# Kernel optimization log

Hardware: AMD Instinct MI355X
Metric: run time of the kernel (lower is better)

Reference implementation:

```python
import jax, jax.numpy as jnp
import numpy as np

N_NODES, N_EDGES, D_IN, D_H, N_GRAPHS = 50000, 600000, 1024, 128, 1000


def _transformer_conv(x, src, dst, wq, bq, wk, bk, wv, bv, ws, bs, n):
    """PyG TransformerConv, heads=1, concat=True, root_weight=True."""
    q = x @ wq + bq                      # [N, d]
    k = x @ wk + bk
    v = x @ wv + bv
    d = q.shape[-1]
    # per-edge attention score for edge j->i: <q_i, k_j> / sqrt(d)
    score = jnp.sum(q[dst] * k[src], axis=-1) / jnp.sqrt(jnp.asarray(d, x.dtype))  # [E]
    # segment softmax over incoming edges of each destination node
    smax = jax.ops.segment_max(score, dst, num_segments=n)
    smax = jnp.where(jnp.isfinite(smax), smax, jnp.zeros_like(smax))
    ex = jnp.exp(score - smax[dst])
    denom = jax.ops.segment_sum(ex, dst, num_segments=n)
    alpha = ex / (denom[dst] + 1e-16)
    # scatter-aggregate weighted values back to destination nodes
    agg = jax.ops.segment_sum(alpha[:, None] * v[src], dst, num_segments=n)  # [N, d]
    # skip (root) connection
    return agg + x @ ws + bs


def setup_inputs() -> dict:
    key = jax.random.key(0)
    ks = jax.random.split(key, 20)
    inp = {}
    inp['x'] = jax.random.normal(ks[0], (N_NODES, D_IN), dtype=jnp.float32)
    inp['edge_index'] = jax.random.randint(ks[1], (2, N_EDGES), 0, N_NODES, dtype=jnp.int64)
    inp['idx'] = jax.random.randint(ks[2], (N_GRAPHS,), 0, N_NODES, dtype=jnp.int64)
    s_in = 0.02
    # layer 0: 1024 -> 128
    for i, nm in enumerate(['wq0', 'wk0', 'wv0', 'ws0']):
        inp[nm] = jax.random.normal(ks[3 + i], (D_IN, D_H), dtype=jnp.float32) * s_in
    for nm in ['bq0', 'bk0', 'bv0', 'bs0']:
        inp[nm] = jnp.zeros((D_H,), dtype=jnp.float32)
    # layer 1: 128 -> 128
    for i, nm in enumerate(['wq1', 'wk1', 'wv1', 'ws1']):
        inp[nm] = jax.random.normal(ks[7 + i], (D_H, D_H), dtype=jnp.float32) * 0.08
    for nm in ['bq1', 'bk1', 'bv1', 'bs1']:
        inp[nm] = jnp.zeros((D_H,), dtype=jnp.float32)
    # MLP head 128 -> 128 -> 64 -> 1
    inp['mw1'] = jax.random.normal(ks[11], (D_H, D_H), dtype=jnp.float32) * 0.08
    inp['mb1'] = jnp.zeros((D_H,), dtype=jnp.float32)
    inp['mw2'] = jax.random.normal(ks[12], (D_H, 64), dtype=jnp.float32) * 0.08
    inp['mb2'] = jnp.zeros((64,), dtype=jnp.float32)
    inp['mw3'] = jax.random.normal(ks[13], (64, 1), dtype=jnp.float32) * 0.1
    inp['mb3'] = jnp.zeros((1,), dtype=jnp.float32)
    return inp


def reference(x, edge_index, idx,
              wq0, bq0, wk0, bk0, wv0, bv0, ws0, bs0,
              wq1, bq1, wk1, bk1, wv1, bv1, ws1, bs1,
              mw1, mb1, mw2, mb2, mw3, mb3):
    src, dst = edge_index[0], edge_index[1]
    n = x.shape[0]
    h = _transformer_conv(x, src, dst, wq0, bq0, wk0, bk0, wv0, bv0, ws0, bs0, n)
    h = jax.nn.relu(h)
    h = _transformer_conv(h, src, dst, wq1, bq1, wk1, bk1, wv1, bv1, ws1, bs1, n)
    h = jax.nn.relu(h)
    h = h[idx]                           # one center node per graph -> [B, d]
    h = jax.nn.relu(h @ mw1 + mb1)       # dropout is identity in eval
    h = jax.nn.relu(h @ mw2 + mb2)
    out = jax.nn.sigmoid(h @ mw3 + mb3)  # [B, 1]
    return out
```

## Files before the change

### kernel.cpp

```cpp
#include <hip/hip_runtime.h>
#include <hip/hip_bf16.h>
#include <cstdint>
#include <cstddef>

typedef __bf16 bf16x2 __attribute__((ext_vector_type(2)));
typedef __bf16 bf16x8 __attribute__((ext_vector_type(8)));
typedef float f32x4 __attribute__((ext_vector_type(4)));

__device__ __forceinline__ void gl_lds16(const __bf16* g, __bf16* l) {
    __builtin_amdgcn_global_load_lds(
        (const __attribute__((address_space(1))) unsigned int*)g,
        (__attribute__((address_space(3))) unsigned int*)l, 16, 0, 0);
}

template <typename AT>
__device__ __forceinline__ bf16x8 loadA8(const AT* p) {
    if constexpr (sizeof(AT) == 4) {
        float4 u = *(const float4*)p;
        float4 v = *(const float4*)(p + 4);
        return (bf16x8){(__bf16)u.x, (__bf16)u.y, (__bf16)u.z, (__bf16)u.w,
                        (__bf16)v.x, (__bf16)v.y, (__bf16)v.z, (__bf16)v.w};
    } else {
        return *(const bf16x8*)p;
    }
}

__global__ __launch_bounds__(256) void mark_idx_kernel(const int* __restrict__ idx,
                                                       int* __restrict__ flagIdx,
                                                       int* __restrict__ flagU, int B) {
    int t = blockIdx.x * 256 + threadIdx.x;
    if (t < B) {
        int n = idx[t];
        flagIdx[n] = 1;
        flagU[n] = 1;
    }
}

__global__ __launch_bounds__(256) void hist_mark_kernel(const int* __restrict__ esrc,
                                                        const int* __restrict__ edst,
                                                        const int* __restrict__ flagIdx,
                                                        int* __restrict__ deg,
                                                        int* __restrict__ flagU, int E) {
    int e = blockIdx.x * 256 + threadIdx.x;
    if (e < E) {
        int d = edst[e];
        atomicAdd(&deg[d], 1);
        if (flagIdx[d]) flagU[esrc[e]] = 1;
    }
}

__global__ __launch_bounds__(1024) void scan8_kernel(const int* __restrict__ deg,
                                                     int* __restrict__ off, int n,
                                                     const int* __restrict__ flagU,
                                                     int* __restrict__ U,
                                                     int* __restrict__ nU) {
    __shared__ int wsum[16];
    int tid = threadIdx.x, lane = tid & 63, wid = tid >> 6;
    if (tid == 0) off[0] = 0;
    int carry = 0;
    int nchunk = (n + 8191) >> 13;
    for (int c = 0; c < nchunk; ++c) {
        int base = (c << 13) + tid * 8;
        int4 a = *(const int4*)(deg + base);
        int4 b = *(const int4*)(deg + base + 4);
        int s[8];
        s[0] = a.x; s[1] = s[0] + a.y; s[2] = s[1] + a.z; s[3] = s[2] + a.w;
        s[4] = s[3] + b.x; s[5] = s[4] + b.y; s[6] = s[5] + b.z; s[7] = s[6] + b.w;
        int x = s[7];
        for (int o = 1; o < 64; o <<= 1) {
            int t = __shfl_up(x, o, 64);
            if (lane >= o) x += t;
        }
        if (lane == 63) wsum[wid] = x;
        __syncthreads();
        if (wid == 0 && lane < 16) {
            int w = wsum[lane];
            for (int o = 1; o < 16; o <<= 1) {
                int t = __shfl_up(w, o, 64);
                if (lane >= o) w += t;
            }
            wsum[lane] = w;
        }
        __syncthreads();
        int pre = carry + (wid ? wsum[wid - 1] : 0) + (x - s[7]);
#pragma unroll
        for (int i = 0; i < 8; ++i)
            if (base + i < n) off[base + i + 1] = pre + s[i];
        carry += wsum[15];
        __syncthreads();
    }
    for (int i = tid; i < n; i += 1024)
        if (flagU[i]) U[atomicAdd(nU, 1)] = i;
}

__global__ __launch_bounds__(256) void scatter_kernel(const int* __restrict__ src,
                                                      const int* __restrict__ dst,
                                                      const int* __restrict__ off,
                                                      int* __restrict__ cursor,
                                                      int* __restrict__ srcs, int E) {
    int e = blockIdx.x * 256 + threadIdx.x;
    if (e < E) {
        int d = dst[e];
        int p = off[d] + atomicAdd(&cursor[d], 1);
        srcs[p] = src[e];
    }
}

__global__ __launch_bounds__(256) void pack_w_kernel(const float* __restrict__ wq0, const float* __restrict__ wk0,
                                                     const float* __restrict__ wv0, const float* __restrict__ ws0,
                                                     const float* __restrict__ wq1, const float* __restrict__ wk1,
                                                     const float* __restrict__ wv1, const float* __restrict__ ws1,
                                                     const float* __restrict__ bq0, const float* __restrict__ bk0,
                                                     const float* __restrict__ bv0, const float* __restrict__ bs0,
                                                     const float* __restrict__ bq1, const float* __restrict__ bk1,
                                                     const float* __restrict__ bv1, const float* __restrict__ bs1,
                                                     __bf16* __restrict__ w0t, __bf16* __restrict__ w1t,
                                                     float* __restrict__ b0, float* __restrict__ b1) {
    int i = blockIdx.x * 256 + threadIdx.x;
    const int S0 = 512 * 1024, S1 = 512 * 128;
    if (i < S0) {
        int n = i >> 10, k = i & 1023;
        int sel = n >> 7, c = n & 127;
        const float* w = (sel == 0) ? wk0 : (sel == 1) ? wv0 : (sel == 2) ? wq0 : ws0;
        w0t[i] = (__bf16)w[(size_t)k * 128 + c];
    } else if (i < S0 + S1) {
        int j = i - S0;
        int n = j >> 7, k = j & 127;
        int sel = n >> 7, c = n & 127;
        const float* w = (sel == 0) ? wk1 : (sel == 1) ? wv1 : (sel == 2) ? wq1 : ws1;
        w1t[j] = (__bf16)w[(size_t)k * 128 + c];
    } else if (i < S0 + S1 + 512) {
        int t = i - S0 - S1;
        int sel = t >> 7, c = t & 127;
        const float* b = (sel == 0) ? bk0 : (sel == 1) ? bv0 : (sel == 2) ? bq0 : bs0;
        b0[t] = b[c];
    } else if (i < S0 + S1 + 1024) {
        int t = i - S0 - S1 - 512;
        int sel = t >> 7, c = t & 127;
        const float* b = (sel == 0) ? bk1 : (sel == 1) ? bv1 : (sel == 2) ? bq1 : bs1;
        b1[t] = b[c];
    }
}

template <typename AT>
__global__ __launch_bounds__(512) void gemm_dual_kernel(const AT* __restrict__ A,
                                                        const __bf16* __restrict__ Bt,
                                                        const float* __restrict__ bias,
                                                        __bf16* __restrict__ outb,
                                                        float* __restrict__ outf,
                                                        const int* __restrict__ rl0,
                                                        const int* __restrict__ np0, int ns0,
                                                        const int* __restrict__ rl1,
                                                        const int* __restrict__ np1, int ns1,
                                                        int K) {
    __shared__ __align__(16) __bf16 Asl[128 * 32];
    __shared__ __align__(16) __bf16 Bsl[128 * 32];
    const int sector = blockIdx.x >> 1;
    const int nbase = (blockIdx.x & 1) << 7;
    const int* rowlist = sector ? rl1 : rl0;
    const int* nptr = sector ? np1 : np0;
    const int nrows = nptr ? *nptr : (sector ? ns1 : ns0);
    if (nrows <= 0) return;
    const __bf16* BT = Bt + (size_t)(sector ? 256 : 0) * K;
    const float* bs = bias + (sector ? 256 : 0);
    const int ntiles = (nrows + 127) >> 7;

    const int tid = threadIdx.x;
    const int lane = tid & 63, wid = tid >> 6;
    const int wm = wid >> 2, wn = wid & 3;
    const int fr = lane & 15, quad = lane >> 4;
    const int rr = tid >> 2;
    const int kc8 = (tid & 3) << 3;

    const __bf16* gB = BT + (size_t)(nbase + rr) * K + kc8;
    __bf16* ldsB = Bsl + (size_t)(wid << 4) * 32;

    for (int mt = blockIdx.y; mt < ntiles; mt += gridDim.y) {
        const int mbase = mt << 7;
        int lr = mbase + rr;
        if (lr >= nrows) lr = nrows - 1;
        const int gr = rowlist ? rowlist[lr] : lr;
        const AT* gA = A + (size_t)gr * K + kc8;

        f32x4 acc[4][2];
#pragma unroll
        for (int i = 0; i < 4; i++)
#pragma unroll
            for (int j = 0; j < 2; j++) acc[i][j] = (f32x4){0.f, 0.f, 0.f, 0.f};

        for (int k0 = 0; k0 < K; k0 += 32) {
            __syncthreads();
            gl_lds16(gB + k0, ldsB);
            bf16x8 a8 = loadA8(gA + k0);
            *(bf16x8*)&Asl[rr * 32 + kc8] = a8;
            __syncthreads();
            bf16x8 af[4], bfr[2];
#pragma unroll
            for (int mi = 0; mi < 4; mi++)
                af[mi] = *(const bf16x8*)&Asl[(wm * 64 + mi * 16 + fr) * 32 + quad * 8];
#pragma unroll
            for (int ni = 0; ni < 2; ni++)
                bfr[ni] = *(const bf16x8*)&Bsl[(wn * 32 + ni * 16 + fr) * 32 + quad * 8];
#pragma unroll
            for (int mi = 0; mi < 4; mi++)
#pragma unroll
                for (int ni = 0; ni < 2; ni++)
                    acc[mi][ni] = __builtin_amdgcn_mfma_f32_16x16x32_bf16(af[mi], bfr[ni], acc[mi][ni], 0, 0, 0);
        }

#pragma unroll
        for (int mi = 0; mi < 4; mi++)
#pragma unroll
            for (int ni = 0; ni < 2; ni++) {
                int rl = wm * 64 + mi * 16 + quad * 4;
                int cl = wn * 32 + ni * 16 + fr;
                float b = bs[nbase + cl];
                int gcol = nbase + cl;
#pragma unroll
                for (int r = 0; r < 4; r++) {
                    int lr2 = mbase + rl + r;
                    if (lr2 < nrows) {
                        int gr2 = rowlist ? rowlist[lr2] : lr2;
                        float v = acc[mi][ni][r] + b;
                        if (sector == 0) outb[(size_t)gr2 * 256 + gcol] = (__bf16)v;
                        else             outf[(size_t)gr2 * 256 + gcol] = v;
                    }
                }
            }
        __syncthreads();
    }
}

__global__ __launch_bounds__(256) void attn_kernel(const float* __restrict__ qs,
                                                   const __bf16* __restrict__ kvb,
                                                   const int* __restrict__ off,
                                                   const int* __restrict__ srcs,
                                                   const int* __restrict__ nodelist,
                                                   const int* __restrict__ nptr, int nstatic,
                                                   __bf16* __restrict__ outb,
                                                   float* __restrict__ outf, int mode) {
    int n = nptr ? *nptr : nstatic;
    int lane = threadIdx.x & 63;
    int w0 = blockIdx.x * 4 + (threadIdx.x >> 6);
    int nw = gridDim.x * 4;
    const float scale = 0.08838834764831845f;
    for (int w = w0; w < n; w += nw) {
        int node = nodelist ? nodelist[w] : w;
        const float* bq = qs + (size_t)node * 256;
        float2 q = *(const float2*)(bq + 2 * lane);
        float2 s = *(const float2*)(bq + 128 + 2 * lane);
        int e0 = off[node], e1 = off[node + 1];
        float m = -INFINITY, l = 0.f;
        float ax = 0.f, ay = 0.f;
        bf16x2 kc = {(__bf16)0.f, (__bf16)0.f}, vc = kc;
        if (e0 < e1) {
            const __bf16* p = kvb + (size_t)srcs[e0] * 256;
            kc = *(const bf16x2*)(p + 2 * lane);
            vc = *(const bf16x2*)(p + 128 + 2 * lane);
        }
        for (int e = e0; e < e1; ++e) {
            bf16x2 kn = {(__bf16)0.f, (__bf16)0.f}, vn = kn;
            if (e + 1 < e1) {
                const __bf16* p = kvb + (size_t)srcs[e + 1] * 256;
                kn = *(const bf16x2*)(p + 2 * lane);
                vn = *(const bf16x2*)(p + 128 + 2 * lane);
            }
            float t = q.x * (float)kc.x + q.y * (float)kc.y;
#pragma unroll
            for (int o = 32; o > 0; o >>= 1) t += __shfl_xor(t, o, 64);
            float sc = t * scale;
            float mn = fmaxf(m, sc);
            float al = __expf(m - mn);
            float ee = __expf(sc - mn);
            ax = ax * al + ee * (float)vc.x;
            ay = ay * al + ee * (float)vc.y;
            l = l * al + ee;
            m = mn;
            kc = kn; vc = vn;
        }
        float inv = 1.f / (l + 1e-16f);
        float ox = ax * inv + s.x, oy = ay * inv + s.y;
        if (mode) {
            bf16x2 o2 = {(__bf16)fmaxf(ox, 0.f), (__bf16)fmaxf(oy, 0.f)};
            *(bf16x2*)(outb + (size_t)node * 128 + 2 * lane) = o2;
        } else {
            float2 o2 = {fmaxf(ox, 0.f), fmaxf(oy, 0.f)};
            *(float2*)(outf + (size_t)w * 128 + 2 * lane) = o2;
        }
    }
}

__global__ __launch_bounds__(128) void mlp_kernel(const float* __restrict__ hbuf,
                                                  const float* __restrict__ mw1, const float* __restrict__ mb1,
                                                  const float* __restrict__ mw2, const float* __restrict__ mb2,
                                                  const float* __restrict__ mw3, const float* __restrict__ mb3,
                                                  float* __restrict__ out, int B) {
    int b = blockIdx.x;
    int t = threadIdx.x;
    if (b >= B) return;
    __shared__ float xr[128], z1[128], z2[64];
    xr[t] = hbuf[(size_t)b * 128 + t];
    __syncthreads();
    float a1 = mb1[t];
#pragma unroll 8
    for (int k = 0; k < 128; ++k) a1 += xr[k] * mw1[k * 128 + t];
    z1[t] = fmaxf(a1, 0.f);
    __syncthreads();
    if (t < 64) {
        float a2 = mb2[t];
#pragma unroll 8
        for (int k = 0; k < 128; ++k) a2 += z1[k] * mw2[k * 64 + t];
        z2[t] = fmaxf(a2, 0.f);
    }
    __syncthreads();
    if (t < 64) {
        float p = z2[t] * mw3[t];
#pragma unroll
        for (int o = 32; o > 0; o >>= 1) p += __shfl_xor(p, o, 64);
        if (t == 0) out[b] = 1.f / (1.f + __expf(-(p + mb3[0])));
    }
}

extern "C" void kernel_launch(void* const* d_in, const int* in_sizes, int n_in,
                              void* d_out, int out_size, void* d_ws, size_t ws_size,
                              hipStream_t stream) {
    const float* x   = (const float*)d_in[0];
    const int*   ei  = (const int*)d_in[1];
    const int*   idx = (const int*)d_in[2];
    const float* wq0 = (const float*)d_in[3];
    const float* wk0 = (const float*)d_in[4];
    const float* wv0 = (const float*)d_in[5];
    const float* ws0 = (const float*)d_in[6];
    const float* bq0 = (const float*)d_in[7];
    const float* bk0 = (const float*)d_in[8];
    const float* bv0 = (const float*)d_in[9];
    const float* bs0 = (const float*)d_in[10];
    const float* wq1 = (const float*)d_in[11];
    const float* wk1 = (const float*)d_in[12];
    const float* wv1 = (const float*)d_in[13];
    const float* ws1 = (const float*)d_in[14];
    const float* bq1 = (const float*)d_in[15];
    const float* bk1 = (const float*)d_in[16];
    const float* bv1 = (const float*)d_in[17];
    const float* bs1 = (const float*)d_in[18];
    const float* mw1 = (const float*)d_in[19];
    const float* mb1 = (const float*)d_in[20];
    const float* mw2 = (const float*)d_in[21];
    const float* mb2 = (const float*)d_in[22];
    const float* mw3 = (const float*)d_in[23];
    const float* mb3 = (const float*)d_in[24];
    float* out = (float*)d_out;

    const int Nn = in_sizes[0] / 1024;
    const int E  = in_sizes[1] / 2;
    const int B  = in_sizes[2];
    const int* esrc = ei;
    const int* edst = ei + E;
    const int degPad = ((Nn + 8191) >> 13) << 13;

    uintptr_t base = (uintptr_t)d_ws;
    auto alloc = [&](size_t bytes) -> void* {
        uintptr_t p = (base + 255) & ~(uintptr_t)255;
        base = p + bytes;
        return (void*)p;
    };
    __bf16* kvb  = (__bf16*)alloc((size_t)Nn * 256 * 2);
    __bf16* kv1b = kvb;
    float*  qs   = (float*)alloc((size_t)Nn * 256 * 4);
    float*  qs1  = qs;
    __bf16* h0b  = (__bf16*)alloc((size_t)Nn * 128 * 2);
    float*  hbuf = (float*)alloc((size_t)B * 128 * 4);
    __bf16* w0t  = (__bf16*)alloc(512 * 1024 * 2);
    __bf16* w1t  = (__bf16*)alloc(512 * 128 * 2);
    float*  b0   = (float*)alloc(512 * 4);
    float*  b1   = (float*)alloc(512 * 4);
    int* deg     = (int*)alloc((size_t)degPad * 4);
    int* cursor  = (int*)alloc((size_t)Nn * 4);
    int* flagIdx = (int*)alloc((size_t)Nn * 4);
    int* flagU   = (int*)alloc((size_t)Nn * 4);
    int* nU      = (int*)alloc(256);
    size_t zbytes = (uintptr_t)nU + 256 - (uintptr_t)deg;
    int* off     = (int*)alloc((size_t)(Nn + 1) * 4);
    int* srcs    = (int*)alloc((size_t)E * 4);
    int* U       = (int*)alloc((size_t)Nn * 4);

    hipMemsetAsync(deg, 0, zbytes, stream);

    mark_idx_kernel<<<(B + 255) / 256, 256, 0, stream>>>(idx, flagIdx, flagU, B);
    hist_mark_kernel<<<(E + 255) / 256, 256, 0, stream>>>(esrc, edst, flagIdx, deg, flagU, E);
    scan8_kernel<<<1, 1024, 0, stream>>>(deg, off, Nn, flagU, U, nU);
    scatter_kernel<<<(E + 255) / 256, 256, 0, stream>>>(esrc, edst, off, cursor, srcs, E);

    pack_w_kernel<<<(512 * 1024 + 512 * 128 + 1024 + 255) / 256, 256, 0, stream>>>(
        wq0, wk0, wv0, ws0, wq1, wk1, wv1, ws1,
        bq0, bk0, bv0, bs0, bq1, bk1, bv1, bs1, w0t, w1t, b0, b1);

    const int mtiles = (Nn + 127) / 128;

    gemm_dual_kernel<float><<<dim3(4, mtiles), 512, 0, stream>>>(x, w0t, b0, kvb, qs,
                                                                 nullptr, nullptr, Nn,
                                                                 U, nU, 0, 1024);
    attn_kernel<<<4096, 256, 0, stream>>>(qs, kvb, off, srcs, U, nU, 0, h0b, nullptr, 1);

    gemm_dual_kernel<__bf16><<<dim3(4, 96), 512, 0, stream>>>(h0b, w1t, b1, kv1b, qs1,
                                                              U, nU, 0,
                                                              idx, nullptr, B, 128);
    attn_kernel<<<(B + 3) / 4, 256, 0, stream>>>(qs1, kv1b, off, srcs, idx, nullptr, B, nullptr, hbuf, 0);

    mlp_kernel<<<B, 128, 0, stream>>>(hbuf, mw1, mb1, mw2, mb2, mw3, mb3, out, B);
}
```

Measured before the change: 637.8 us.

## Widen GEMM tile to 128x256 and double-buffer LDS with prefetch

```diff
diff --git a/kernel.cpp b/kernel.cpp
--- a/kernel.cpp
+++ b/kernel.cpp
@@ -143,20 +143,19 @@
 }
 
 template <typename AT>
-__global__ __launch_bounds__(512) void gemm_dual_kernel(const AT* __restrict__ A,
-                                                        const __bf16* __restrict__ Bt,
-                                                        const float* __restrict__ bias,
-                                                        __bf16* __restrict__ outb,
-                                                        float* __restrict__ outf,
-                                                        const int* __restrict__ rl0,
-                                                        const int* __restrict__ np0, int ns0,
-                                                        const int* __restrict__ rl1,
-                                                        const int* __restrict__ np1, int ns1,
-                                                        int K) {
-    __shared__ __align__(16) __bf16 Asl[128 * 32];
-    __shared__ __align__(16) __bf16 Bsl[128 * 32];
-    const int sector = blockIdx.x >> 1;
-    const int nbase = (blockIdx.x & 1) << 7;
+__global__ __launch_bounds__(512, 4) void gemm_dual_kernel(const AT* __restrict__ A,
+                                                           const __bf16* __restrict__ Bt,
+                                                           const float* __restrict__ bias,
+                                                           __bf16* __restrict__ outb,
+                                                           float* __restrict__ outf,
+                                                           const int* __restrict__ rl0,
+                                                           const int* __restrict__ np0, int ns0,
+                                                           const int* __restrict__ rl1,
+                                                           const int* __restrict__ np1, int ns1,
+                                                           int K) {
+    __shared__ __align__(16) __bf16 Asl[2][128 * 32];
+    __shared__ __align__(16) __bf16 Bsl[2][256 * 32];
+    const int sector = blockIdx.x;
     const int* rowlist = sector ? rl1 : rl0;
     const int* nptr = sector ? np1 : np0;
     const int nrows = nptr ? *nptr : (sector ? ns1 : ns0);
@@ -172,8 +171,7 @@
     const int rr = tid >> 2;
     const int kc8 = (tid & 3) << 3;
 
-    const __bf16* gB = BT + (size_t)(nbase + rr) * K + kc8;
-    __bf16* ldsB = Bsl + (size_t)(wid << 4) * 32;
+    const __bf16* gB = BT + (size_t)rr * K + kc8;
 
     for (int mt = blockIdx.y; mt < ntiles; mt += gridDim.y) {
         const int mbase = mt << 7;
@@ -182,52 +180,70 @@
         const int gr = rowlist ? rowlist[lr] : lr;
         const AT* gA = A + (size_t)gr * K + kc8;
 
-        f32x4 acc[4][2];
+        f32x4 acc[4][4];
 #pragma unroll
         for (int i = 0; i < 4; i++)
 #pragma unroll
-            for (int j = 0; j < 2; j++) acc[i][j] = (f32x4){0.f, 0.f, 0.f, 0.f};
-
+            for (int j = 0; j < 4; j++) acc[i][j] = (f32x4){0.f, 0.f, 0.f, 0.f};
+
+        __syncthreads();
+        {
+            __bf16* bd = &Bsl[0][(wid << 4) * 32];
+            gl_lds16(gB, bd);
+            gl_lds16(gB + (size_t)128 * K, bd + 128 * 32);
+            bf16x8 a0 = loadA8(gA);
+            *(bf16x8*)&Asl[0][rr * 32 + kc8] = a0;
+        }
+        __syncthreads();
+
+        int cur = 0;
         for (int k0 = 0; k0 < K; k0 += 32) {
-            __syncthreads();
-            gl_lds16(gB + k0, ldsB);
-            bf16x8 a8 = loadA8(gA + k0);
-            *(bf16x8*)&Asl[rr * 32 + kc8] = a8;
-            __syncthreads();
-            bf16x8 af[4], bfr[2];
+            const int kn = k0 + 32;
+            const bool pf = (kn < K);
+            bf16x8 aN;
+            if (pf) {
+                __bf16* bd = &Bsl[cur ^ 1][(wid << 4) * 32];
+                gl_lds16(gB + kn, bd);
+                gl_lds16(gB + (size_t)128 * K + kn, bd + 128 * 32);
+                aN = loadA8(gA + kn);
+            }
+            bf16x8 af[4], bfr[4];
 #pragma unroll
             for (int mi = 0; mi < 4; mi++)
-                af[mi] = *(const bf16x8*)&Asl[(wm * 64 + mi * 16 + fr) * 32 + quad * 8];
-#pragma unroll
-            for (int ni = 0; ni < 2; ni++)
-                bfr[ni] = *(const bf16x8*)&Bsl[(wn * 32 + ni * 16 + fr) * 32 + quad * 8];
+                af[mi] = *(const bf16x8*)&Asl[cur][(wm * 64 + mi * 16 + fr) * 32 + quad * 8];
+#pragma unroll
+            for (int ni = 0; ni < 4; ni++)
+                bfr[ni] = *(const bf16x8*)&Bsl[cur][(wn * 64 + ni * 16 + fr) * 32 + quad * 8];
 #pragma unroll
             for (int mi = 0; mi < 4; mi++)
 #pragma unroll
-                for (int ni = 0; ni < 2; ni++)
+                for (int ni = 0; ni < 4; ni++)
                     acc[mi][ni] = __builtin_amdgcn_mfma_f32_16x16x32_bf16(af[mi], bfr[ni], acc[mi][ni], 0, 0, 0);
+            if (pf) {
+                *(bf16x8*)&Asl[cur ^ 1][rr * 32 + kc8] = aN;
+                __syncthreads();
+            }
+            cur ^= 1;
         }
 
 #pragma unroll
         for (int mi = 0; mi < 4; mi++)
 #pragma unroll
-            for (int ni = 0; ni < 2; ni++) {
+            for (int ni = 0; ni < 4; ni++) {
                 int rl = wm * 64 + mi * 16 + quad * 4;
-                int cl = wn * 32 + ni * 16 + fr;
-                float b = bs[nbase + cl];
-                int gcol = nbase + cl;
+                int cl = wn * 64 + ni * 16 + fr;
+                float b = bs[cl];
 #pragma unroll
                 for (int r = 0; r < 4; r++) {
                     int lr2 = mbase + rl + r;
                     if (lr2 < nrows) {
                         int gr2 = rowlist ? rowlist[lr2] : lr2;
                         float v = acc[mi][ni][r] + b;
-                        if (sector == 0) outb[(size_t)gr2 * 256 + gcol] = (__bf16)v;
-                        else             outf[(size_t)gr2 * 256 + gcol] = v;
+                        if (sector == 0) outb[(size_t)gr2 * 256 + cl] = (__bf16)v;
+                        else             outf[(size_t)gr2 * 256 + cl] = v;
                     }
                 }
             }
-        __syncthreads();
     }
 }
 
@@ -397,14 +413,14 @@
 
     const int mtiles = (Nn + 127) / 128;
 
-    gemm_dual_kernel<float><<<dim3(4, mtiles), 512, 0, stream>>>(x, w0t, b0, kvb, qs,
+    gemm_dual_kernel<float><<<dim3(2, mtiles), 512, 0, stream>>>(x, w0t, b0, kvb, qs,
                                                                  nullptr, nullptr, Nn,
                                                                  U, nU, 0, 1024);
     attn_kernel<<<4096, 256, 0, stream>>>(qs, kvb, off, srcs, U, nU, 0, h0b, nullptr, 1);
 
-    gemm_dual_kernel<__bf16><<<dim3(4, 96), 512, 0, stream>>>(h0b, w1t, b1, kv1b, qs1,
-                                                              U, nU, 0,
-                                                              idx, nullptr, B, 128);
+    gemm_dual_kernel<__bf16><<<dim3(2, 128), 512, 0, stream>>>(h0b, w1t, b1, kv1b, qs1,
+                                                               U, nU, 0,
+                                                               idx, nullptr, B, 128);
     attn_kernel<<<(B + 3) / 4, 256, 0, stream>>>(qs1, kv1b, off, srcs, idx, nullptr, B, nullptr, hbuf, 0);
 
     mlp_kernel<<<B, 128, 0, stream>>>(hbuf, mw1, mb1, mw2, mb2, mw3, mb3, out, B);
```

Measured after the change: 651.4 us. 1.02x slower.
